# Kernel optimization log

Hardware: AMD Instinct MI355X
Metric: run time of the kernel (lower is better)

Reference implementation:

```python
import jax, jax.numpy as jnp
import numpy as np

N_THETA, N_GAMMA, HIDDEN = 16, 64, 64
SCENE_DIM, QUERY_DIM = 16, 60
B, N_OBJ = 65536, 10
N_STEPS, DT = 20, 0.01
K_THETA, K_GAMMA, K_CROSS = 1.0, 1.0, 0.5
TWO_PI = 2.0 * np.pi


def setup_inputs() -> dict:
    key = jax.random.key(0)
    ks = jax.random.split(key, 10)
    scene = jax.random.normal(ks[0], (B, N_OBJ, SCENE_DIM), jnp.float32)
    query = jax.random.normal(ks[1], (B, QUERY_DIM), jnp.float32)
    # per-sample seeded initial oscillator state (batched)
    theta_phase0 = jax.random.uniform(ks[2], (B, N_THETA), jnp.float32, 0.0, TWO_PI)
    gamma_phase0 = jax.random.uniform(ks[3], (B, N_GAMMA), jnp.float32, 0.0, TWO_PI)
    theta_freq = TWO_PI * (4.0 + 4.0 * jax.random.uniform(ks[4], (B, N_THETA), jnp.float32))   # theta band 4-8 Hz
    gamma_freq = TWO_PI * (30.0 + 50.0 * jax.random.uniform(ks[5], (B, N_GAMMA), jnp.float32))  # gamma band 30-80 Hz
    init = lambda k, shp, fan: (jax.random.normal(k, shp, jnp.float32) / np.sqrt(fan)).astype(jnp.float32)
    Ws = init(ks[6], (SCENE_DIM, N_GAMMA), SCENE_DIM)
    bs = jnp.zeros((N_GAMMA,), jnp.float32)
    Wq = init(ks[7], (QUERY_DIM, HIDDEN), QUERY_DIM)
    bq = jnp.zeros((HIDDEN,), jnp.float32)
    d_comb = N_THETA + N_GAMMA + HIDDEN  # 144
    W1 = init(ks[8], (d_comb, HIDDEN), d_comb)
    b1 = jnp.zeros((HIDDEN,), jnp.float32)
    W2 = init(ks[9], (HIDDEN, 2), HIDDEN)
    b2 = jnp.zeros((2,), jnp.float32)
    return {"scene": scene, "query": query,
            "theta_phase0": theta_phase0, "theta_freq": theta_freq,
            "gamma_phase0": gamma_phase0, "gamma_freq": gamma_freq,
            "Ws": Ws, "bs": bs, "Wq": Wq, "bq": bq,
            "W1": W1, "b1": b1, "W2": W2, "b2": b2}


def _integrate(theta_phase0, theta_amp0, theta_freq, gamma_phase0, gamma_amp0, gamma_freq):
    """Batched Euler integration of theta-gamma Kuramoto network.

    Mean-field all-to-all coupling: sum_j a_j*sin(p_j - p_i)
      = cos(p_i)*sum_j a_j*sin(p_j) - sin(p_i)*sum_j a_j*cos(p_j).
    """
    def step(carry, _):
        tp, ta, gp, ga = carry  # (B,Nt),(B,Nt),(B,Ng),(B,Ng)
        st, ct = jnp.sin(tp), jnp.cos(tp)
        sg, cg = jnp.sin(gp), jnp.cos(gp)
        # theta intra-population coupling (amplitude-weighted mean field)
        Ti = jnp.sum(ta * st, -1, keepdims=True)
        Tr = jnp.sum(ta * ct, -1, keepdims=True)
        coup_t = (Ti * ct - Tr * st) / N_THETA
        # gamma intra-population coupling
        Gi = jnp.sum(ga * sg, -1, keepdims=True)
        Gr = jnp.sum(ga * cg, -1, keepdims=True)
        coup_g = (Gi * cg - Gr * sg) / N_GAMMA
        # theta -> gamma cross-frequency phase coupling (mean theta field)
        mi = jnp.mean(st, -1, keepdims=True)
        mr = jnp.mean(ct, -1, keepdims=True)
        cross = mi * cg - mr * sg
        dtp = theta_freq + K_THETA * coup_t
        dgp = gamma_freq + K_GAMMA * coup_g + K_CROSS * cross
        dta = ta * (1.0 - ta * ta)   # Stuart-Landau amplitude dynamics
        dga = ga * (1.0 - ga * ga)
        new = (tp + DT * dtp, ta + DT * dta, gp + DT * dgp, ga + DT * dga)
        return new, None

    carry0 = (theta_phase0, theta_amp0, gamma_phase0, gamma_amp0)
    (tp, ta, gp, ga), _ = jax.lax.scan(step, carry0, None, length=N_STEPS)
    return tp, ta, gp, ga


def reference(scene, query, theta_phase0, theta_freq, gamma_phase0, gamma_freq,
              Ws, bs, Wq, bq, W1, b1, W2, b2):
    scene_flat = jnp.mean(scene, axis=1)                      # (B, D_scene)
    gamma_init = jax.nn.sigmoid(scene_flat @ Ws + bs)         # (B, n_gamma)
    gamma_amp0 = jax.lax.stop_gradient(gamma_init)            # .detach() in original
    theta_amp0 = jnp.ones_like(theta_phase0)
    _, ta, _, ga = _integrate(theta_phase0, theta_amp0, theta_freq,
                              gamma_phase0, gamma_amp0, gamma_freq)
    osc_feat = jnp.concatenate([ta, ga], axis=-1)             # (B, n_theta+n_gamma)
    q_feat = query @ Wq + bq                                  # (B, hidden)
    combined = jnp.concatenate([osc_feat, q_feat], axis=-1)   # (B, 144)
    h = jax.nn.relu(combined @ W1 + b1)
    logits = h @ W2 + b2
    return jax.nn.log_softmax(logits, axis=-1)
```

## Files before the change

kernel.cpp:

```cpp
#include <hip/hip_runtime.h>


typedef __fp16 h2_t  __attribute__((ext_vector_type(2)));
typedef __fp16 f16x4 __attribute__((ext_vector_type(4)));
typedef __fp16 f16x8 __attribute__((ext_vector_type(8)));
typedef float  f32x4 __attribute__((ext_vector_type(4)));
typedef unsigned u32x4 __attribute__((ext_vector_type(4)));

union H2U { unsigned u; h2_t h; };
union F4  { unsigned u[2]; f16x4 h; };
union F8  { u32x4 u; f16x8 h; };

__device__ __forceinline__ unsigned pk(float a, float b) {
    H2U v; v.h = __builtin_amdgcn_cvt_pkrtz(a, b);
    return v.u;
}
__device__ __forceinline__ float F20(float g) {
    #pragma unroll
    for (int n = 0; n < 20; ++n) {
        float g2 = g * g;
        g = fmaf(0.01f, g * (1.0f - g2), g);
    }
    return g;
}

#define WHo   0
#define WQTo  2048
#define WS2o  4128
#define LUTo  4640
#define BSo   4900
#define BSUMo 4964
#define W2o   5028
#define SFTo  5156
#define QTo   5668
#define LDSW  (QTo + 32 * 66)

__global__ __launch_bounds__(256, 4) void fused_kernel(
    const float* __restrict__ scene,
    const float* __restrict__ query,
    const float* __restrict__ Ws,
    const float* __restrict__ bs,
    const float* __restrict__ Wq,
    const float* __restrict__ bq,
    const float* __restrict__ W1,
    const float* __restrict__ b1,
    const float* __restrict__ W2,
    const float* __restrict__ b2,
    float* __restrict__ out)
{
    __shared__ __align__(16) unsigned lds[LDSW];
    float* ldsF = (float*)lds;
    const int t    = threadIdx.x;
    const int lane = t & 63;
    const int wv   = __builtin_amdgcn_readfirstlane(t) >> 6;
    const int kb   = lane >> 4;
    const int jw   = lane & 15;
    const int eb   = blockIdx.x << 6;

    F8 aWq[4][2];
    #pragma unroll
    for (int dt = 0; dt < 4; ++dt) {
        const int d = (dt << 4) + jw;
        #pragma unroll
        for (int kk = 0; kk < 2; ++kk) {
            const int c0 = (kk << 5) + (kb << 3);
            float4 lo = {0.f,0.f,0.f,0.f}, hi = {0.f,0.f,0.f,0.f};
            if (d < 60) {
                lo = *(const float4*)(Wq + d * 64 + c0);
                hi = *(const float4*)(Wq + d * 64 + c0 + 4);
            } else if (d == 60) {
                lo = *(const float4*)(bq + c0);
                hi = *(const float4*)(bq + c0 + 4);
            }
            F8 f;
            f.u[0] = pk(lo.x, lo.y); f.u[1] = pk(lo.z, lo.w);
            f.u[2] = pk(hi.x, hi.y); f.u[3] = pk(hi.z, hi.w);
            aWq[dt][kk] = f;
        }
    }

    {
        const int j = lane;
        #pragma unroll
        for (int ii = 0; ii < 2; ++ii) {
            const int ch = (wv << 1) + ii;
            u32x4 v;
            #pragma unroll
            for (int pp = 0; pp < 4; ++pp) {
                const int p  = (ch << 2) + pp;
                const int g0 = (((p >> 4) << 1) + ((p & 3) >> 1)) * 16
                             + (((p >> 2) & 3) << 2) + ((p & 1) << 1);
                v[pp] = pk(W1[(16 + g0) * 64 + j], W1[(17 + g0) * 64 + j]);
            }
            *(u32x4*)&lds[WHo + (j << 5) + ((ch ^ (j & 7)) << 2)] = v;
        }
        #pragma unroll
        for (int ii = 0; ii < 8; ++ii) {
            const int cp = (wv << 3) + ii;
            lds[WQTo + cp * 65 + j] =
                pk(W1[(80 + 2 * cp) * 64 + j], W1[(81 + 2 * cp) * 64 + j]);
        }
    }
    #pragma unroll
    for (int ii = 0; ii < 2; ++ii) {
        const int w = t + (ii << 8);
        const int dp = w >> 6, g = w & 63;
        lds[WS2o + w] = pk(0.1f * Ws[(2 * dp) * 64 + g],
                           0.1f * Ws[(2 * dp + 1) * 64 + g]);
    }
    {
        float x0 = (float)t * 0.03125f - 4.0f;
        ldsF[LUTo + t] = F20(1.0f / (1.0f + __expf(-x0)));
        if (t == 0) ldsF[LUTo + 256] = F20(1.0f / (1.0f + __expf(-4.0f)));
    }
    if (t < 64) {
        float s = b1[t];
        #pragma unroll
        for (int r = 0; r < 16; ++r) s += W1[r * 64 + t];
        ldsF[BSUMo + t] = s;
    } else if (t < 128) {
        ldsF[BSo + (t - 64)] = bs[t - 64];
    } else {
        ldsF[W2o + (t - 128)] = W2[t - 128];
    }
    const int sel = t >> 2, q4 = t & 3;
    {
        const float4* sp = (const float4*)scene + (size_t)(eb + sel) * 40 + q4;
        float4 a = sp[0];
        #pragma unroll
        for (int o = 1; o < 10; ++o) {
            float4 v = sp[4 * o];
            a.x += v.x; a.y += v.y; a.z += v.z; a.w += v.w;
        }
        lds[SFTo + ((q4 << 1) + 0) * 64 + sel] = pk(a.x, a.y);
        lds[SFTo + ((q4 << 1) + 1) * 64 + sel] = pk(a.z, a.w);
    }
    #pragma unroll
    for (int i = 0; i < 4; ++i) {
        const int idx = t + (i << 8);
        if (idx < 960) {
            const int qel = idx / 15, aq = idx - qel * 15;
            float4 qv = ((const float4*)query)[(size_t)(eb + qel) * 15 + aq];
            const int p0 = ((aq >> 3) << 4) + ((aq & 3) << 2) + (((aq >> 2) & 1) << 1);
            lds[QTo + (p0 + 0) * 66 + qel] = pk(qv.x, qv.y);
            lds[QTo + (p0 + 1) * 66 + qel] = pk(qv.z, qv.w);
        }
    }
    if (t < 64)       lds[QTo + 30 * 66 + t]        = pk(1.0f, 0.0f);
    else if (t < 128) lds[QTo + 31 * 66 + (t - 64)] = 0u;
    __syncthreads();

    const int q   = jw;
    const int elb = ((t >> 6) << 4) | q;

    F4 bsf;
    bsf.u[0] = lds[SFTo + (2 * kb + 0) * 64 + elb];
    bsf.u[1] = lds[SFTo + (2 * kb + 1) * 64 + elb];
    f32x4 xs[4];
    #pragma unroll
    for (int tt = 0; tt < 4; ++tt) {
        F4 aW;
        aW.u[0] = lds[WS2o + (2 * kb + 0) * 64 + tt * 16 + q];
        aW.u[1] = lds[WS2o + (2 * kb + 1) * 64 + tt * 16 + q];
        f32x4 cinit = *(const f32x4*)&ldsF[BSo + tt * 16 + (kb << 2)];
        xs[tt] = __builtin_amdgcn_mfma_f32_16x16x16f16(aW.h, bsf.h, cinit, 0, 0, 0);
    }
    auto GA = [&](float x) -> float {
        float u = fminf(fmaxf(fmaf(x, 32.0f, 128.0f), 0.0f), 255.999f);
        int   i0 = (int)u;
        float f0 = ldsF[LUTo + i0], f1 = ldsF[LUTo + i0 + 1];
        return fmaf(u - (float)i0, f1 - f0, f0);
    };
    F8 bfrag[4];
    #pragma unroll
    for (int c = 0; c < 2; ++c) {
        F8 f;
        f.u[0] = pk(GA(xs[2 * c][0]),     GA(xs[2 * c][1]));
        f.u[1] = pk(GA(xs[2 * c][2]),     GA(xs[2 * c][3]));
        f.u[2] = pk(GA(xs[2 * c + 1][0]), GA(xs[2 * c + 1][1]));
        f.u[3] = pk(GA(xs[2 * c + 1][2]), GA(xs[2 * c + 1][3]));
        bfrag[c] = f;
    }
    #pragma unroll
    for (int c2 = 0; c2 < 2; ++c2) {
        F8 f;
        #pragma unroll
        for (int r = 0; r < 4; ++r)
            f.u[r] = lds[QTo + ((kb << 2) + r + (c2 << 4)) * 66 + elb];
        bfrag[2 + c2] = f;
    }

    float l0 = 0.f, l1 = 0.f;
    #pragma unroll
    for (int jt = 0; jt < 4; ++jt) {
        const int j = (jt << 4) | q;
        F8 Bk[2];
        #pragma unroll
        for (int kk = 0; kk < 2; ++kk) {
            F8 f;
            #pragma unroll
            for (int r = 0; r < 4; ++r)
                f.u[r] = lds[WQTo + ((kk << 4) + (kb << 2) + r) * 65 + j];
            Bk[kk] = f;
        }
        const float bsv = ldsF[BSUMo + j];
        F8 qA[2];
        #pragma unroll
        for (int half = 0; half < 2; ++half) {
            f32x4 accT[2];
            #pragma unroll
            for (int dd = 0; dd < 2; ++dd) {
                const int dt = (half << 1) + dd;
                f32x4 c0 = {0.f, 0.f, 0.f, 0.f};
                if (dt == 3) c0[0] = (kb == 3) ? bsv : 0.f;
                f32x4 a1 = __builtin_amdgcn_mfma_f32_16x16x32_f16(
                               aWq[dt][0].h, Bk[0].h, c0, 0, 0, 0);
                accT[dd] = __builtin_amdgcn_mfma_f32_16x16x32_f16(
                               aWq[dt][1].h, Bk[1].h, a1, 0, 0, 0);
            }
            F8 f;
            f.u[0] = pk(accT[0][0], accT[0][1]);
            f.u[1] = pk(accT[0][2], accT[0][3]);
            f.u[2] = pk(accT[1][0], accT[1][1]);
            f.u[3] = pk(accT[1][2], accT[1][3]);
            qA[half] = f;
        }
        f32x4 hacc = {0.f, 0.f, 0.f, 0.f};
        #pragma unroll
        for (int c = 0; c < 2; ++c) {
            const int ch = ((c << 2) | kb) ^ (j & 7);
            F8 a;
            a.u = *(const u32x4*)&lds[WHo + (j << 5) + (ch << 2)];
            hacc = __builtin_amdgcn_mfma_f32_16x16x32_f16(a.h, bfrag[c].h, hacc, 0, 0, 0);
        }
        hacc = __builtin_amdgcn_mfma_f32_16x16x32_f16(qA[0].h, bfrag[2].h, hacc, 0, 0, 0);
        hacc = __builtin_amdgcn_mfma_f32_16x16x32_f16(qA[1].h, bfrag[3].h, hacc, 0, 0, 0);
        #pragma unroll
        for (int r = 0; r < 4; ++r) {
            const int jr = (jt << 4) + (kb << 2) + r;
            float hv = fmaxf(hacc[r], 0.f);
            float2 wv2 = *(const float2*)&ldsF[W2o + (jr << 1)];
            l0 = fmaf(hv, wv2.x, l0);
            l1 = fmaf(hv, wv2.y, l1);
        }
    }
    l0 += __shfl_xor(l0, 16); l0 += __shfl_xor(l0, 32);
    l1 += __shfl_xor(l1, 16); l1 += __shfl_xor(l1, 32);
    l0 += b2[0]; l1 += b2[1];
    if (lane < 16) {
        const float mx = fmaxf(l0, l1);
        const float lz = mx + __logf(__expf(l0 - mx) + __expf(l1 - mx));
        float2 o = { l0 - lz, l1 - lz };
        ((float2*)out)[eb + elb] = o;
    }
}

extern "C" void kernel_launch(void* const* d_in, const int* in_sizes, int n_in,
                              void* d_out, int out_size, void* d_ws, size_t ws_size,
                              hipStream_t stream) {
    const float* scene = (const float*)d_in[0];
    const float* query = (const float*)d_in[1];
    const float* Ws = (const float*)d_in[6];
    const float* bs = (const float*)d_in[7];
    const float* Wq = (const float*)d_in[8];
    const float* bq = (const float*)d_in[9];
    const float* W1 = (const float*)d_in[10];
    const float* b1 = (const float*)d_in[11];
    const float* W2 = (const float*)d_in[12];
    const float* b2 = (const float*)d_in[13];
    float* out = (float*)d_out;

    const int B = in_sizes[0] / 160;
    fused_kernel<<<B / 64, 256, 0, stream>>>(scene, query, Ws, bs, Wq, bq,
                                             W1, b1, W2, b2, out);
}
```

Baseline: 22.23 us.

## Process two 64-sample groups per block with prefetched second-group loads

Each block now handles 128 samples as two groups of 64. The global loads for both groups are issued early, and the second group's loads overlap with the first group's compute through double-buffered LDS activation regions. The per-block setup cost (weight packing, LUT build, Wq fragments) is spread over twice as many samples. In exchange, register pressure rises from holding 14 extra float4 prefetch values, launch bounds drop from 4 to 3 blocks per SM, and the grid is halved, which may reduce latency hiding.

```diff
diff --git a/kernel.cpp b/kernel.cpp
--- a/kernel.cpp
+++ b/kernel.cpp
@@ -31,11 +31,12 @@
 #define BSo   4900
 #define BSUMo 4964
 #define W2o   5028
-#define SFTo  5156
-#define QTo   5668
-#define LDSW  (QTo + 32 * 66)
-
-__global__ __launch_bounds__(256, 4) void fused_kernel(
+#define ACT0  5156
+#define ACT1  7780
+#define ACTW  2624
+#define LDSW  (ACT1 + ACTW)
+
+__global__ __launch_bounds__(256, 3) void fused_kernel(
     const float* __restrict__ scene,
     const float* __restrict__ query,
     const float* __restrict__ Ws,
@@ -55,7 +56,44 @@
     const int wv   = __builtin_amdgcn_readfirstlane(t) >> 6;
     const int kb   = lane >> 4;
     const int jw   = lane & 15;
-    const int eb   = blockIdx.x << 6;
+    const int eb   = blockIdx.x << 7;
+    const int sel  = t >> 2, q4 = t & 3;
+
+    auto issueLoads = [&](int gbase, float4 (&sv)[10], float4 (&qv)[4]) {
+        const float4* sp = (const float4*)scene + (size_t)(gbase + sel) * 40 + q4;
+        #pragma unroll
+        for (int o = 0; o < 10; ++o) sv[o] = sp[4 * o];
+        #pragma unroll
+        for (int i = 0; i < 4; ++i) {
+            const int idx = t + (i << 8);
+            if (idx < 960) {
+                const int qel = idx / 15, aq = idx - qel * 15;
+                qv[i] = ((const float4*)query)[(size_t)(gbase + qel) * 15 + aq];
+            }
+        }
+    };
+    auto writeActs = [&](unsigned* A, const float4 (&sv)[10], const float4 (&qv)[4]) {
+        float4 a = sv[0];
+        #pragma unroll
+        for (int o = 1; o < 10; ++o) {
+            a.x += sv[o].x; a.y += sv[o].y; a.z += sv[o].z; a.w += sv[o].w;
+        }
+        A[((q4 << 1) + 0) * 64 + sel] = pk(a.x, a.y);
+        A[((q4 << 1) + 1) * 64 + sel] = pk(a.z, a.w);
+        #pragma unroll
+        for (int i = 0; i < 4; ++i) {
+            const int idx = t + (i << 8);
+            if (idx < 960) {
+                const int qel = idx / 15, aq = idx - qel * 15;
+                const int p0 = ((aq >> 3) << 4) + ((aq & 3) << 2) + (((aq >> 2) & 1) << 1);
+                A[512 + (p0 + 0) * 66 + qel] = pk(qv[i].x, qv[i].y);
+                A[512 + (p0 + 1) * 66 + qel] = pk(qv[i].z, qv[i].w);
+            }
+        }
+    };
+
+    float4 sv0[10], qv0[4];
+    issueLoads(eb, sv0, qv0);
 
     F8 aWq[4][2];
     #pragma unroll
@@ -123,136 +161,130 @@
     } else {
         ldsF[W2o + (t - 128)] = W2[t - 128];
     }
-    const int sel = t >> 2, q4 = t & 3;
-    {
-        const float4* sp = (const float4*)scene + (size_t)(eb + sel) * 40 + q4;
-        float4 a = sp[0];
-        #pragma unroll
-        for (int o = 1; o < 10; ++o) {
-            float4 v = sp[4 * o];
-            a.x += v.x; a.y += v.y; a.z += v.z; a.w += v.w;
-        }
-        lds[SFTo + ((q4 << 1) + 0) * 64 + sel] = pk(a.x, a.y);
-        lds[SFTo + ((q4 << 1) + 1) * 64 + sel] = pk(a.z, a.w);
-    }
-    #pragma unroll
-    for (int i = 0; i < 4; ++i) {
-        const int idx = t + (i << 8);
-        if (idx < 960) {
-            const int qel = idx / 15, aq = idx - qel * 15;
-            float4 qv = ((const float4*)query)[(size_t)(eb + qel) * 15 + aq];
-            const int p0 = ((aq >> 3) << 4) + ((aq & 3) << 2) + (((aq >> 2) & 1) << 1);
-            lds[QTo + (p0 + 0) * 66 + qel] = pk(qv.x, qv.y);
-            lds[QTo + (p0 + 1) * 66 + qel] = pk(qv.z, qv.w);
-        }
-    }
-    if (t < 64)       lds[QTo + 30 * 66 + t]        = pk(1.0f, 0.0f);
-    else if (t < 128) lds[QTo + 31 * 66 + (t - 64)] = 0u;
+    writeActs(&lds[ACT0], sv0, qv0);
+    if (t < 64) {
+        lds[ACT0 + 512 + 30 * 66 + t] = pk(1.0f, 0.0f);
+        lds[ACT1 + 512 + 30 * 66 + t] = pk(1.0f, 0.0f);
+    } else if (t < 128) {
+        lds[ACT0 + 512 + 31 * 66 + (t - 64)] = 0u;
+        lds[ACT1 + 512 + 31 * 66 + (t - 64)] = 0u;
+    }
     __syncthreads();
+
+    float4 sv1[10], qv1[4];
+    issueLoads(eb + 64, sv1, qv1);
 
     const int q   = jw;
     const int elb = ((t >> 6) << 4) | q;
 
-    F4 bsf;
-    bsf.u[0] = lds[SFTo + (2 * kb + 0) * 64 + elb];
-    bsf.u[1] = lds[SFTo + (2 * kb + 1) * 64 + elb];
-    f32x4 xs[4];
-    #pragma unroll
-    for (int tt = 0; tt < 4; ++tt) {
-        F4 aW;
-        aW.u[0] = lds[WS2o + (2 * kb + 0) * 64 + tt * 16 + q];
-        aW.u[1] = lds[WS2o + (2 * kb + 1) * 64 + tt * 16 + q];
-        f32x4 cinit = *(const f32x4*)&ldsF[BSo + tt * 16 + (kb << 2)];
-        xs[tt] = __builtin_amdgcn_mfma_f32_16x16x16f16(aW.h, bsf.h, cinit, 0, 0, 0);
-    }
-    auto GA = [&](float x) -> float {
-        float u = fminf(fmaxf(fmaf(x, 32.0f, 128.0f), 0.0f), 255.999f);
-        int   i0 = (int)u;
-        float f0 = ldsF[LUTo + i0], f1 = ldsF[LUTo + i0 + 1];
-        return fmaf(u - (float)i0, f1 - f0, f0);
+    auto computeGroup = [&](const unsigned* A, int ebase) {
+        F4 bsf;
+        bsf.u[0] = A[(2 * kb + 0) * 64 + elb];
+        bsf.u[1] = A[(2 * kb + 1) * 64 + elb];
+        f32x4 xs[4];
+        #pragma unroll
+        for (int tt = 0; tt < 4; ++tt) {
+            F4 aW;
+            aW.u[0] = lds[WS2o + (2 * kb + 0) * 64 + tt * 16 + q];
+            aW.u[1] = lds[WS2o + (2 * kb + 1) * 64 + tt * 16 + q];
+            f32x4 cinit = *(const f32x4*)&ldsF[BSo + tt * 16 + (kb << 2)];
+            xs[tt] = __builtin_amdgcn_mfma_f32_16x16x16f16(aW.h, bsf.h, cinit, 0, 0, 0);
+        }
+        auto GA = [&](float x) -> float {
+            float u = fminf(fmaxf(fmaf(x, 32.0f, 128.0f), 0.0f), 255.999f);
+            int   i0 = (int)u;
+            float f0 = ldsF[LUTo + i0], f1 = ldsF[LUTo + i0 + 1];
+            return fmaf(u - (float)i0, f1 - f0, f0);
+        };
+        F8 bfrag[4];
+        #pragma unroll
+        for (int c = 0; c < 2; ++c) {
+            F8 f;
+            f.u[0] = pk(GA(xs[2 * c][0]),     GA(xs[2 * c][1]));
+            f.u[1] = pk(GA(xs[2 * c][2]),     GA(xs[2 * c][3]));
+            f.u[2] = pk(GA(xs[2 * c + 1][0]), GA(xs[2 * c + 1][1]));
+            f.u[3] = pk(GA(xs[2 * c + 1][2]), GA(xs[2 * c + 1][3]));
+            bfrag[c] = f;
+        }
+        #pragma unroll
+        for (int c2 = 0; c2 < 2; ++c2) {
+            F8 f;
+            #pragma unroll
+            for (int r = 0; r < 4; ++r)
+                f.u[r] = A[512 + ((kb << 2) + r + (c2 << 4)) * 66 + elb];
+            bfrag[2 + c2] = f;
+        }
+
+        float l0 = 0.f, l1 = 0.f;
+        #pragma unroll
+        for (int jt = 0; jt < 4; ++jt) {
+            const int j = (jt << 4) | q;
+            F8 Bk[2];
+            #pragma unroll
+            for (int kk = 0; kk < 2; ++kk) {
+                F8 f;
+                #pragma unroll
+                for (int r = 0; r < 4; ++r)
+                    f.u[r] = lds[WQTo + ((kk << 4) + (kb << 2) + r) * 65 + j];
+                Bk[kk] = f;
+            }
+            const float bsv = ldsF[BSUMo + j];
+            F8 qA[2];
+            #pragma unroll
+            for (int half = 0; half < 2; ++half) {
+                f32x4 accT[2];
+                #pragma unroll
+                for (int dd = 0; dd < 2; ++dd) {
+                    const int dt = (half << 1) + dd;
+                    f32x4 c0 = {0.f, 0.f, 0.f, 0.f};
+                    if (dt == 3) c0[0] = (kb == 3) ? bsv : 0.f;
+                    f32x4 a1 = __builtin_amdgcn_mfma_f32_16x16x32_f16(
+                                   aWq[dt][0].h, Bk[0].h, c0, 0, 0, 0);
+                    accT[dd] = __builtin_amdgcn_mfma_f32_16x16x32_f16(
+                                   aWq[dt][1].h, Bk[1].h, a1, 0, 0, 0);
+                }
+                F8 f;
+                f.u[0] = pk(accT[0][0], accT[0][1]);
+                f.u[1] = pk(accT[0][2], accT[0][3]);
+                f.u[2] = pk(accT[1][0], accT[1][1]);
+                f.u[3] = pk(accT[1][2], accT[1][3]);
+                qA[half] = f;
+            }
+            f32x4 hacc = {0.f, 0.f, 0.f, 0.f};
+            #pragma unroll
+            for (int c = 0; c < 2; ++c) {
+                const int ch = ((c << 2) | kb) ^ (j & 7);
+                F8 a;
+                a.u = *(const u32x4*)&lds[WHo + (j << 5) + (ch << 2)];
+                hacc = __builtin_amdgcn_mfma_f32_16x16x32_f16(a.h, bfrag[c].h, hacc, 0, 0, 0);
+            }
+            hacc = __builtin_amdgcn_mfma_f32_16x16x32_f16(qA[0].h, bfrag[2].h, hacc, 0, 0, 0);
+            hacc = __builtin_amdgcn_mfma_f32_16x16x32_f16(qA[1].h, bfrag[3].h, hacc, 0, 0, 0);
+            #pragma unroll
+            for (int r = 0; r < 4; ++r) {
+                const int jr = (jt << 4) + (kb << 2) + r;
+                float hv = fmaxf(hacc[r], 0.f);
+                float2 wv2 = *(const float2*)&ldsF[W2o + (jr << 1)];
+                l0 = fmaf(hv, wv2.x, l0);
+                l1 = fmaf(hv, wv2.y, l1);
+            }
+        }
+        l0 += __shfl_xor(l0, 16); l0 += __shfl_xor(l0, 32);
+        l1 += __shfl_xor(l1, 16); l1 += __shfl_xor(l1, 32);
+        l0 += b2[0]; l1 += b2[1];
+        if (lane < 16) {
+            const float mx = fmaxf(l0, l1);
+            const float lz = mx + __logf(__expf(l0 - mx) + __expf(l1 - mx));
+            float2 o = { l0 - lz, l1 - lz };
+            ((float2*)out)[ebase + elb] = o;
+        }
     };
-    F8 bfrag[4];
-    #pragma unroll
-    for (int c = 0; c < 2; ++c) {
-        F8 f;
-        f.u[0] = pk(GA(xs[2 * c][0]),     GA(xs[2 * c][1]));
-        f.u[1] = pk(GA(xs[2 * c][2]),     GA(xs[2 * c][3]));
-        f.u[2] = pk(GA(xs[2 * c + 1][0]), GA(xs[2 * c + 1][1]));
-        f.u[3] = pk(GA(xs[2 * c + 1][2]), GA(xs[2 * c + 1][3]));
-        bfrag[c] = f;
-    }
-    #pragma unroll
-    for (int c2 = 0; c2 < 2; ++c2) {
-        F8 f;
-        #pragma unroll
-        for (int r = 0; r < 4; ++r)
-            f.u[r] = lds[QTo + ((kb << 2) + r + (c2 << 4)) * 66 + elb];
-        bfrag[2 + c2] = f;
-    }
-
-    float l0 = 0.f, l1 = 0.f;
-    #pragma unroll
-    for (int jt = 0; jt < 4; ++jt) {
-        const int j = (jt << 4) | q;
-        F8 Bk[2];
-        #pragma unroll
-        for (int kk = 0; kk < 2; ++kk) {
-            F8 f;
-            #pragma unroll
-            for (int r = 0; r < 4; ++r)
-                f.u[r] = lds[WQTo + ((kk << 4) + (kb << 2) + r) * 65 + j];
-            Bk[kk] = f;
-        }
-        const float bsv = ldsF[BSUMo + j];
-        F8 qA[2];
-        #pragma unroll
-        for (int half = 0; half < 2; ++half) {
-            f32x4 accT[2];
-            #pragma unroll
-            for (int dd = 0; dd < 2; ++dd) {
-                const int dt = (half << 1) + dd;
-                f32x4 c0 = {0.f, 0.f, 0.f, 0.f};
-                if (dt == 3) c0[0] = (kb == 3) ? bsv : 0.f;
-                f32x4 a1 = __builtin_amdgcn_mfma_f32_16x16x32_f16(
-                               aWq[dt][0].h, Bk[0].h, c0, 0, 0, 0);
-                accT[dd] = __builtin_amdgcn_mfma_f32_16x16x32_f16(
-                               aWq[dt][1].h, Bk[1].h, a1, 0, 0, 0);
-            }
-            F8 f;
-            f.u[0] = pk(accT[0][0], accT[0][1]);
-            f.u[1] = pk(accT[0][2], accT[0][3]);
-            f.u[2] = pk(accT[1][0], accT[1][1]);
-            f.u[3] = pk(accT[1][2], accT[1][3]);
-            qA[half] = f;
-        }
-        f32x4 hacc = {0.f, 0.f, 0.f, 0.f};
-        #pragma unroll
-        for (int c = 0; c < 2; ++c) {
-            const int ch = ((c << 2) | kb) ^ (j & 7);
-            F8 a;
-            a.u = *(const u32x4*)&lds[WHo + (j << 5) + (ch << 2)];
-            hacc = __builtin_amdgcn_mfma_f32_16x16x32_f16(a.h, bfrag[c].h, hacc, 0, 0, 0);
-        }
-        hacc = __builtin_amdgcn_mfma_f32_16x16x32_f16(qA[0].h, bfrag[2].h, hacc, 0, 0, 0);
-        hacc = __builtin_amdgcn_mfma_f32_16x16x32_f16(qA[1].h, bfrag[3].h, hacc, 0, 0, 0);
-        #pragma unroll
-        for (int r = 0; r < 4; ++r) {
-            const int jr = (jt << 4) + (kb << 2) + r;
-            float hv = fmaxf(hacc[r], 0.f);
-            float2 wv2 = *(const float2*)&ldsF[W2o + (jr << 1)];
-            l0 = fmaf(hv, wv2.x, l0);
-            l1 = fmaf(hv, wv2.y, l1);
-        }
-    }
-    l0 += __shfl_xor(l0, 16); l0 += __shfl_xor(l0, 32);
-    l1 += __shfl_xor(l1, 16); l1 += __shfl_xor(l1, 32);
-    l0 += b2[0]; l1 += b2[1];
-    if (lane < 16) {
-        const float mx = fmaxf(l0, l1);
-        const float lz = mx + __logf(__expf(l0 - mx) + __expf(l1 - mx));
-        float2 o = { l0 - lz, l1 - lz };
-        ((float2*)out)[eb + elb] = o;
-    }
+
+    computeGroup(&lds[ACT0], eb);
+
+    writeActs(&lds[ACT1], sv1, qv1);
+    __syncthreads();
+    computeGroup(&lds[ACT1], eb + 64);
 }
 
 extern "C" void kernel_launch(void* const* d_in, const int* in_sizes, int n_in,
@@ -271,6 +303,6 @@
     float* out = (float*)d_out;
 
     const int B = in_sizes[0] / 160;
-    fused_kernel<<<B / 64, 256, 0, stream>>>(scene, query, Ws, bs, Wq, bq,
-                                             W1, b1, W2, b2, out);
+    fused_kernel<<<B / 128, 256, 0, stream>>>(scene, query, Ws, bs, Wq, bq,
+                                              W1, b1, W2, b2, out);
 }
```

After: 29.99 us. +34.9%, slower.
